# Kernel optimization log

Measured on AMD Instinct MI355X. Metric: run time of the kernel, lower is better.

The kernel has to match this reference:

```python
import jax, jax.numpy as jnp
import numpy as np

N = 100000
E = 500000
HID = 256
N_EDGE_TYPES = 5
N_ATOM = 16
N_CHARGE = 7
NUM_RBF = 16
CUTOFF = 5.0
LN_EPS = 1e-5


def _xavier(key, shape):
    fan_in, fan_out = shape[0], shape[1]
    lim = float(np.sqrt(6.0 / (fan_in + fan_out)))
    return jax.random.uniform(key, shape, jnp.float32, -lim, lim)


def setup_inputs() -> dict:
    key = jax.random.key(0)
    ks = jax.random.split(key, 12)
    input_dim = HID * 2 + NUM_RBF + N_ATOM + N_CHARGE  # 551
    h = jax.random.normal(ks[0], (N, HID), jnp.float32)
    x = jax.random.normal(ks[1], (N, 3), jnp.float32)
    spawn_node_idx = jax.random.randint(ks[2], (E,), 0, N)
    existing_node_idx = jax.random.randint(ks[3], (E,), 0, N)
    ins_x = jax.random.normal(ks[4], (E, 3), jnp.float32)
    ins_a = jax.random.randint(ks[5], (E,), 0, N_ATOM)
    ins_c = jax.random.randint(ks[6], (E,), 0, N_CHARGE)
    # MLP params (Xavier weights, zero biases; LayerNorm gamma=1, beta=0)
    W1 = _xavier(ks[7], (input_dim, HID)); b1 = jnp.zeros((HID,), jnp.float32)
    g1 = jnp.ones((HID,), jnp.float32); be1 = jnp.zeros((HID,), jnp.float32)
    W2 = _xavier(ks[8], (HID, HID // 2)); b2 = jnp.zeros((HID // 2,), jnp.float32)
    g2 = jnp.ones((HID // 2,), jnp.float32); be2 = jnp.zeros((HID // 2,), jnp.float32)
    W3 = _xavier(ks[9], (HID // 2, N_EDGE_TYPES)); b3 = jnp.zeros((N_EDGE_TYPES,), jnp.float32)
    # Gaussian RBF parameters: centers on [0, cutoff], shared width from spacing
    rbf_mu = jnp.linspace(0.0, CUTOFF, NUM_RBF).astype(jnp.float32)
    delta = CUTOFF / (NUM_RBF - 1)
    rbf_gamma = jnp.asarray(1.0 / (2.0 * delta * delta), jnp.float32)
    return {"h": h, "x": x, "spawn_node_idx": spawn_node_idx,
            "existing_node_idx": existing_node_idx, "ins_x": ins_x,
            "ins_a": ins_a, "ins_c": ins_c,
            "W1": W1, "b1": b1, "g1": g1, "be1": be1,
            "W2": W2, "b2": b2, "g2": g2, "be2": be2,
            "W3": W3, "b3": b3, "rbf_mu": rbf_mu, "rbf_gamma": rbf_gamma}


def _layer_norm(z, gamma, beta):
    mu = jnp.mean(z, axis=-1, keepdims=True)
    var = jnp.mean((z - mu) ** 2, axis=-1, keepdims=True)
    return (z - mu) * jax.lax.rsqrt(var + LN_EPS) * gamma + beta


def reference(h, x, spawn_node_idx, existing_node_idx, ins_x, ins_a, ins_c,
              W1, b1, g1, be1, W2, b2, g2, be2, W3, b3, rbf_mu, rbf_gamma):
    # gather node pairs  [E, HID] / [E, 3]
    h_spawn = h[spawn_node_idx]
    h_existing = h[existing_node_idx]
    existing_pos = x[existing_node_idx]
    # distance + Gaussian RBF  [E, NUM_RBF]
    d = jnp.maximum(jnp.linalg.norm(ins_x - existing_pos, axis=-1), 1e-6)
    dist_features = jnp.exp(-rbf_gamma * (d[:, None] - rbf_mu) ** 2)
    # one-hot insertion type features
    ins_atom = jax.nn.one_hot(ins_a, N_ATOM, dtype=h.dtype)
    ins_charge = jax.nn.one_hot(ins_c, N_CHARGE, dtype=h.dtype)
    feats = jnp.concatenate([h_spawn, h_existing, dist_features, ins_atom, ins_charge], axis=-1)
    # 3-layer MLP: Linear -> LN -> SiLU -> Linear -> LN -> SiLU -> Linear
    z = jax.nn.silu(_layer_norm(feats @ W1 + b1, g1, be1))
    z = jax.nn.silu(_layer_norm(z @ W2 + b2, g2, be2))
    return z @ W3 + b3  # [E, N_EDGE_TYPES]
```

## Files before the change

### kernel.cpp

```cpp
#include <hip/hip_runtime.h>
#include <stdint.h>

#define NN 100000
#define EE 500000
#define HIDD 256
#define LN_EPS 1e-5f

typedef _Float16 half8 __attribute__((ext_vector_type(8)));
typedef _Float16 half4 __attribute__((ext_vector_type(4)));
typedef __fp16 fp16x2 __attribute__((ext_vector_type(2)));
typedef float f32x4 __attribute__((ext_vector_type(4)));

__device__ __forceinline__ unsigned short f2h(float f) {
  _Float16 h = (_Float16)f;
  union { _Float16 hh; unsigned short us; } u; u.hh = h;
  return u.us;
}

__device__ __forceinline__ unsigned pkrtz(float a, float b) {
  union { fp16x2 h; unsigned u; } c;
  c.h = __builtin_amdgcn_cvt_pkrtz(a, b);
  return c.u;
}

__device__ __forceinline__ float fast_silu(float y) {
  float e = __expf(-y);
  return y * __builtin_amdgcn_rcpf(1.f + e);
}

__device__ __forceinline__ void g2l16(void* lds, const void* g) {
  __builtin_amdgcn_global_load_lds(
      (const __attribute__((address_space(1))) unsigned int*)g,
      (__attribute__((address_space(3))) unsigned int*)lds, 16, 0, 0);
}

__global__ __launch_bounds__(256) void prep_kern(const float* __restrict__ h,
                                                 const float* __restrict__ W1,
                                                 const float* __restrict__ W2,
                                                 const float* __restrict__ W3,
                                                 unsigned short* __restrict__ hb,
                                                 unsigned short* __restrict__ w1sw,
                                                 unsigned short* __restrict__ w2sw,
                                                 unsigned short* __restrict__ w3sw) {
  int b = blockIdx.x;
  if (b < 712) {
    int t = b * 256 + threadIdx.x;
    if (t < 147456) {
      int chunk = t >> 14, rem = t & 16383;
      int kq = rem >> 11, n = (rem >> 3) & 255, j = rem & 7;
      int k = (chunk << 6) + (kq << 3) + j;
      float v = (k < 551) ? W1[k * 256 + n] : 0.f;
      w1sw[t] = f2h(v);
    } else if (t < 147456 + 32768) {
      int t2 = t - 147456;
      int chunk = t2 >> 13, rem = t2 & 8191;
      int kq = rem >> 10, n = (rem >> 3) & 127, j = rem & 7;
      int k = (chunk << 6) + (kq << 3) + j;
      w2sw[t2] = f2h(W2[k * 128 + n]);
    } else if (t < 147456 + 32768 + 2048) {
      int t3 = t - 180224;
      int kq = t3 >> 7, o = (t3 >> 3) & 15, j = t3 & 7;
      int k = (kq << 3) + j;
      w3sw[t3] = f2h((o < 5) ? W3[k * 5 + o] : 0.f);
    }
  } else {
    int i = ((b - 712) * 256 + threadIdx.x) * 8;
    float4 v0 = *(const float4*)(h + i);
    float4 v1 = *(const float4*)(h + i + 4);
    uint4 u;
    u.x = pkrtz(v0.x, v0.y); u.y = pkrtz(v0.z, v0.w);
    u.z = pkrtz(v1.x, v1.y); u.w = pkrtz(v1.z, v1.w);
    *(uint4*)(hb + i) = u;
  }
}

struct __align__(16) SMem {
  short r1[16384];
  short r2[8192];
  _Float16 b1h[256], g1h[256], be1h[256];
  _Float16 b2h[128], g2h[128], be2h[128];
  float muv[16];
  float b3v[8];
  int spI[64], exI[64];
};

__global__ __launch_bounds__(256, 3)
void edge_head_main(const float* __restrict__ h, const float* __restrict__ x,
                    const int* __restrict__ spawn, const int* __restrict__ exist,
                    const float* __restrict__ insx, const int* __restrict__ insa,
                    const int* __restrict__ insc,
                    const float* __restrict__ b1, const float* __restrict__ g1,
                    const float* __restrict__ be1,
                    const float* __restrict__ b2, const float* __restrict__ g2,
                    const float* __restrict__ be2,
                    const float* __restrict__ b3, const float* __restrict__ mu,
                    const float* __restrict__ gammaP,
                    const unsigned short* __restrict__ w1sw,
                    const unsigned short* __restrict__ w2sw,
                    const unsigned short* __restrict__ w3swg,
                    const unsigned short* __restrict__ hb, int use_hb,
                    float* __restrict__ out) {
  __shared__ SMem sm;
  float* red = (float*)sm.r2;
  const int t = threadIdx.x;
  const int base = blockIdx.x * 64;
  const int lane = t & 63;
  const int wv = t >> 6;
  const int cl = lane & 15;
  const int q = lane >> 4;
  const int sx = (cl & 7) << 3;

  sm.b1h[t] = (_Float16)b1[t]; sm.g1h[t] = (_Float16)g1[t]; sm.be1h[t] = (_Float16)be1[t];
  if (t < 128) { sm.b2h[t] = (_Float16)b2[t]; sm.g2h[t] = (_Float16)g2[t]; sm.be2h[t] = (_Float16)be2[t]; }
  if (t < 16) sm.muv[t] = mu[t];
  if (t < 8) sm.b3v[t] = (t < 5) ? b3[t] : 0.f;
  if (t < 64) {
    int e = base + t; int ec = e < EE ? e : EE - 1;
    sm.spI[t] = spawn[ec]; sm.exI[t] = exist[ec];
  }
  const float gma = gammaP[0];

  __syncthreads();

  int4 f8a = {0,0,0,0}, f8b = {0,0,0,0};
  int k1 = 16, k2 = 32;
  if (t < 64) {
    int e = base + t; int ec = e < EE ? e : EE - 1;
    float ix0 = insx[ec * 3], ix1 = insx[ec * 3 + 1], ix2 = insx[ec * 3 + 2];
    int nd = sm.exI[t];
    float dx = ix0 - x[nd * 3], dy = ix1 - x[nd * 3 + 1], dz = ix2 - x[nd * 3 + 2];
    float d = fmaxf(sqrtf(dx * dx + dy * dy + dz * dz), 1e-6f);
    k1 = 16 + insa[ec]; k2 = 32 + insc[ec];
    float rb[16];
#pragma unroll
    for (int k = 0; k < 16; ++k) { float dd = d - sm.muv[k]; rb[k] = __expf(-gma * dd * dd); }
    uint4 ua, ub;
    ua.x = pkrtz(rb[0], rb[1]);  ua.y = pkrtz(rb[2], rb[3]);
    ua.z = pkrtz(rb[4], rb[5]);  ua.w = pkrtz(rb[6], rb[7]);
    ub.x = pkrtz(rb[8], rb[9]);  ub.y = pkrtz(rb[10], rb[11]);
    ub.z = pkrtz(rb[12], rb[13]); ub.w = pkrtz(rb[14], rb[15]);
    f8a = *(int4*)&ua; f8b = *(int4*)&ub;
  }

  const int row0 = t >> 3, p0 = t & 7;
  const int row1 = row0 + 32;
  const int sw0 = ((p0 ^ (row0 & 7)) << 3);
  const int sw1 = ((p0 ^ (row1 & 7)) << 3);

  int4 pA, pB;
  if (use_hb) {
    pA = *(const int4*)(hb + (size_t)sm.spI[row0] * HIDD + p0 * 8);
    pB = *(const int4*)(hb + (size_t)sm.spI[row1] * HIDD + p0 * 8);
  }

  f32x4 acc[4][4];
#pragma unroll
  for (int i = 0; i < 4; ++i)
#pragma unroll
    for (int j = 0; j < 4; ++j) acc[i][j] = (f32x4){0.f, 0.f, 0.f, 0.f};

  for (int c = 0; c < 9; ++c) {
    __syncthreads();
    const unsigned short* gsrc = w1sw + c * 16384;
#pragma unroll
    for (int i = 0; i < 8; ++i)
      g2l16(&sm.r1[(i * 256 + t) * 8], gsrc + (i * 256 + t) * 8);
    if (c < 8) {
      if (use_hb) {
        *(int4*)&sm.r2[row0 * 64 + sw0] = pA;
        *(int4*)&sm.r2[row1 * 64 + sw1] = pB;
        if (c < 7) {
          const int cn = c + 1;
          const int* sel = (cn < 4) ? sm.spI : sm.exI;
          const int colb = (cn & 3) * 64;
          pA = *(const int4*)(hb + (size_t)sel[row0] * HIDD + colb + p0 * 8);
          pB = *(const int4*)(hb + (size_t)sel[row1] * HIDD + colb + p0 * 8);
        }
      } else {
        const int* sel = (c < 4) ? sm.spI : sm.exI;
        const int colb = (c & 3) * 64;
#pragma unroll
        for (int i = 0; i < 2; ++i) {
          int jj = t + i * 256;
          int row = jj >> 3, p = jj & 7;
          const float* s = h + (size_t)sel[row] * HIDD + colb + p * 8;
          float4 v0 = *(const float4*)s, v1 = *(const float4*)(s + 4);
          uint4 u;
          u.x = pkrtz(v0.x, v0.y); u.y = pkrtz(v0.z, v0.w);
          u.z = pkrtz(v1.x, v1.y); u.w = pkrtz(v1.z, v1.w);
          *(uint4*)&sm.r2[row * 64 + ((p ^ (row & 7)) << 3)] = u;
        }
      }
    } else {
      if (t < 64) {
        short* rp = &sm.r2[t * 64];
        const int sw = t & 7;
#pragma unroll
        for (int g = 0; g < 8; ++g) {
          int4 v = (g == 0) ? f8a : (g == 1) ? f8b : (int4){0,0,0,0};
          *(int4*)&rp[(g ^ sw) * 8] = v;
        }
        rp[((k1 >> 3) ^ sw) * 8 + (k1 & 7)] = (short)0x3C00;
        rp[((k2 >> 3) ^ sw) * 8 + (k2 & 7)] = (short)0x3C00;
      }
    }
    __syncthreads();
#pragma unroll
    for (int ks = 0; ks < 2; ++ks) {
      half8 af[4], bf[4];
#pragma unroll
      for (int i = 0; i < 4; ++i)
        af[i] = *(const half8*)&sm.r1[(ks * 4 + q) * 2048 + (wv * 64 + i * 16 + cl) * 8];
#pragma unroll
      for (int j = 0; j < 4; ++j)
        bf[j] = *(const half8*)&sm.r2[(j * 16 + cl) * 64 + ((ks * 32 + q * 8) ^ sx)];
#pragma unroll
      for (int i = 0; i < 4; ++i)
#pragma unroll
        for (int j = 0; j < 4; ++j)
          acc[i][j] = __builtin_amdgcn_mfma_f32_16x16x32_f16(af[i], bf[j], acc[i][j], 0, 0, 0);
    }
  }

  float bf1[4][4];
#pragma unroll
  for (int i = 0; i < 4; ++i) {
    half4 b4 = *(const half4*)&sm.b1h[wv * 64 + i * 16 + q * 4];
#pragma unroll
    for (int r = 0; r < 4; ++r) bf1[i][r] = (float)b4[r];
  }
  float S1arr[4], Q1arr[4];
#pragma unroll
  for (int j = 0; j < 4; ++j) {
    float S = 0.f, Q = 0.f;
#pragma unroll
    for (int i = 0; i < 4; ++i)
#pragma unroll
      for (int r = 0; r < 4; ++r) {
        float v = acc[i][j][r] + bf1[i][r];
        acc[i][j][r] = v; S += v; Q += v * v;
      }
    S += __shfl_xor(S, 16); S += __shfl_xor(S, 32);
    Q += __shfl_xor(Q, 16); Q += __shfl_xor(Q, 32);
    S1arr[j] = S; Q1arr[j] = Q;
  }
  __syncthreads();
  if (q == 0) {
#pragma unroll
    for (int j = 0; j < 4; ++j) {
      red[wv * 64 + j * 16 + cl] = S1arr[j];
      red[256 + wv * 64 + j * 16 + cl] = Q1arr[j];
    }
  }
  __syncthreads();
  float mean1[4], rstd1[4];
#pragma unroll
  for (int j = 0; j < 4; ++j) {
    int m = j * 16 + cl;
    float S = red[m] + red[64 + m] + red[128 + m] + red[192 + m];
    float Q = red[256 + m] + red[320 + m] + red[384 + m] + red[448 + m];
    float mn = S * (1.f / 256.f);
    mean1[j] = mn;
    rstd1[j] = rsqrtf(Q * (1.f / 256.f) - mn * mn + LN_EPS);
  }
#pragma unroll
  for (int i = 0; i < 4; ++i) {
    half4 g4 = *(const half4*)&sm.g1h[wv * 64 + i * 16 + q * 4];
    half4 e4 = *(const half4*)&sm.be1h[wv * 64 + i * 16 + q * 4];
    float gf[4], ef[4];
#pragma unroll
    for (int r = 0; r < 4; ++r) { gf[r] = (float)g4[r]; ef[r] = (float)e4[r]; }
#pragma unroll
    for (int j = 0; j < 4; ++j) {
      float s0 = fast_silu((acc[i][j][0] - mean1[j]) * rstd1[j] * gf[0] + ef[0]);
      float s1 = fast_silu((acc[i][j][1] - mean1[j]) * rstd1[j] * gf[1] + ef[1]);
      float s2 = fast_silu((acc[i][j][2] - mean1[j]) * rstd1[j] * gf[2] + ef[2]);
      float s3 = fast_silu((acc[i][j][3] - mean1[j]) * rstd1[j] * gf[3] + ef[3]);
      uint2 w; w.x = pkrtz(s0, s1); w.y = pkrtz(s2, s3);
      int m = j * 16 + cl;
      int k0 = wv * 64 + i * 16 + q * 4;
      *(uint2*)&sm.r1[m * 256 + (k0 ^ ((m & 7) << 3))] = w;
    }
  }

  f32x4 acc2[2][4];
#pragma unroll
  for (int i = 0; i < 2; ++i)
#pragma unroll
    for (int j = 0; j < 4; ++j) acc2[i][j] = (f32x4){0.f, 0.f, 0.f, 0.f};
  for (int c2 = 0; c2 < 4; ++c2) {
    __syncthreads();
    const unsigned short* gsrc = w2sw + c2 * 8192;
#pragma unroll
    for (int i = 0; i < 4; ++i)
      g2l16(&sm.r2[(i * 256 + t) * 8], gsrc + (i * 256 + t) * 8);
    __syncthreads();
#pragma unroll
    for (int ks = 0; ks < 2; ++ks) {
      half8 af[2], bf[4];
#pragma unroll
      for (int i = 0; i < 2; ++i)
        af[i] = *(const half8*)&sm.r2[(ks * 4 + q) * 1024 + (wv * 32 + i * 16 + cl) * 8];
#pragma unroll
      for (int j = 0; j < 4; ++j)
        bf[j] = *(const half8*)&sm.r1[(j * 16 + cl) * 256 + ((c2 * 64 + ks * 32 + q * 8) ^ sx)];
#pragma unroll
      for (int i = 0; i < 2; ++i)
#pragma unroll
        for (int j = 0; j < 4; ++j)
          acc2[i][j] = __builtin_amdgcn_mfma_f32_16x16x32_f16(af[i], bf[j], acc2[i][j], 0, 0, 0);
    }
  }
  __syncthreads();

  g2l16(&sm.r1[2048 + t * 8], w3swg + t * 8);

  float bf2[2][4];
#pragma unroll
  for (int i = 0; i < 2; ++i) {
    half4 b4 = *(const half4*)&sm.b2h[wv * 32 + i * 16 + q * 4];
#pragma unroll
    for (int r = 0; r < 4; ++r) bf2[i][r] = (float)b4[r];
  }
  float S2arr[4], Q2arr[4];
#pragma unroll
  for (int j = 0; j < 4; ++j) {
    float S = 0.f, Q = 0.f;
#pragma unroll
    for (int i = 0; i < 2; ++i)
#pragma unroll
      for (int r = 0; r < 4; ++r) {
        float v = acc2[i][j][r] + bf2[i][r];
        acc2[i][j][r] = v; S += v; Q += v * v;
      }
    S += __shfl_xor(S, 16); S += __shfl_xor(S, 32);
    Q += __shfl_xor(Q, 16); Q += __shfl_xor(Q, 32);
    S2arr[j] = S; Q2arr[j] = Q;
  }
  if (q == 0) {
#pragma unroll
    for (int j = 0; j < 4; ++j) {
      red[wv * 64 + j * 16 + cl] = S2arr[j];
      red[256 + wv * 64 + j * 16 + cl] = Q2arr[j];
    }
  }
  __syncthreads();
  float mean2[4], rstd2[4];
#pragma unroll
  for (int j = 0; j < 4; ++j) {
    int m = j * 16 + cl;
    float S = red[m] + red[64 + m] + red[128 + m] + red[192 + m];
    float Q = red[256 + m] + red[320 + m] + red[384 + m] + red[448 + m];
    float mn = S * (1.f / 128.f);
    mean2[j] = mn;
    rstd2[j] = rsqrtf(Q * (1.f / 128.f) - mn * mn + LN_EPS);
  }
  __syncthreads();
#pragma unroll
  for (int i = 0; i < 2; ++i) {
    half4 g4 = *(const half4*)&sm.g2h[wv * 32 + i * 16 + q * 4];
    half4 e4 = *(const half4*)&sm.be2h[wv * 32 + i * 16 + q * 4];
    float gf[4], ef[4];
#pragma unroll
    for (int r = 0; r < 4; ++r) { gf[r] = (float)g4[r]; ef[r] = (float)e4[r]; }
#pragma unroll
    for (int j = 0; j < 4; ++j) {
      float s0 = fast_silu((acc2[i][j][0] - mean2[j]) * rstd2[j] * gf[0] + ef[0]);
      float s1 = fast_silu((acc2[i][j][1] - mean2[j]) * rstd2[j] * gf[1] + ef[1]);
      float s2 = fast_silu((acc2[i][j][2] - mean2[j]) * rstd2[j] * gf[2] + ef[2]);
      float s3 = fast_silu((acc2[i][j][3] - mean2[j]) * rstd2[j] * gf[3] + ef[3]);
      uint2 w; w.x = pkrtz(s0, s1); w.y = pkrtz(s2, s3);
      int m = j * 16 + cl;
      int k0 = wv * 32 + i * 16 + q * 4;
      *(uint2*)&sm.r2[m * 128 + (k0 ^ ((m & 7) << 3))] = w;
    }
  }
  __syncthreads();

  f32x4 a3 = (f32x4){0.f, 0.f, 0.f, 0.f};
  const int m3 = wv * 16 + cl;
  const int sx3 = (m3 & 7) << 3;
#pragma unroll
  for (int ks = 0; ks < 4; ++ks) {
    half8 af = *(const half8*)&sm.r1[2048 + (ks * 4 + q) * 128 + cl * 8];
    half8 bf = *(const half8*)&sm.r2[m3 * 128 + ((ks * 32 + q * 8) ^ sx3)];
    a3 = __builtin_amdgcn_mfma_f32_16x16x32_f16(af, bf, a3, 0, 0, 0);
  }
  int e = base + m3;
  if (e < EE) {
#pragma unroll
    for (int r = 0; r < 4; ++r) {
      int o = q * 4 + r;
      if (o < 5) out[e * 5 + o] = a3[r] + sm.b3v[o];
    }
  }
}

extern "C" void kernel_launch(void* const* d_in, const int* in_sizes, int n_in,
                              void* d_out, int out_size, void* d_ws, size_t ws_size,
                              hipStream_t stream) {
  const float* h    = (const float*)d_in[0];
  const float* x    = (const float*)d_in[1];
  const int* spawn  = (const int*)d_in[2];
  const int* exist  = (const int*)d_in[3];
  const float* insx = (const float*)d_in[4];
  const int* insa   = (const int*)d_in[5];
  const int* insc   = (const int*)d_in[6];
  const float* W1   = (const float*)d_in[7];
  const float* b1   = (const float*)d_in[8];
  const float* g1   = (const float*)d_in[9];
  const float* be1  = (const float*)d_in[10];
  const float* W2   = (const float*)d_in[11];
  const float* b2   = (const float*)d_in[12];
  const float* g2   = (const float*)d_in[13];
  const float* be2  = (const float*)d_in[14];
  const float* W3   = (const float*)d_in[15];
  const float* b3   = (const float*)d_in[16];
  const float* mu   = (const float*)d_in[17];
  const float* gma  = (const float*)d_in[18];

  unsigned short* w1sw = (unsigned short*)d_ws;
  unsigned short* w2sw = w1sw + 147456;
  unsigned short* w3sw = w2sw + 32768;
  unsigned short* hb   = w3sw + 2048;
  const size_t need_hb = 364544ull + (size_t)NN * HIDD * 2ull;
  int use_hb = (ws_size >= need_hb) ? 1 : 0;

  prep_kern<<<use_hb ? 13212 : 712, 256, 0, stream>>>(h, W1, W2, W3, hb, w1sw, w2sw, w3sw);
  edge_head_main<<<7813, 256, 0, stream>>>(h, x, spawn, exist, insx, insa, insc,
                                           b1, g1, be1, b2, g2, be2, b3, mu, gma,
                                           w1sw, w2sw, w3sw, hb, use_hb,
                                           (float*)d_out);
}
```

Before: 463.2 us.

## Load MLP weights directly into registers and double-buffer gathered features in LDS

The swizzled fp16 weights for layers 1, 2 and 3 are now loaded straight from global memory into register fragments rather than staged through LDS with global_load_lds. The layer-1 weight chunk is prefetched one iteration ahead. The gathered activation tiles are double-buffered in LDS so there is one barrier per chunk instead of two. Barriers are replaced by a custom lgkmcnt-wait plus s_barrier macro, and LDS use shrinks because the second buffer is no longer needed. In exchange, every wave re-reads weights from global memory or L2 and register pressure rises under the 3-block occupancy target.

```diff
diff --git a/kernel.cpp b/kernel.cpp
--- a/kernel.cpp
+++ b/kernel.cpp
@@ -11,6 +11,8 @@
 typedef __fp16 fp16x2 __attribute__((ext_vector_type(2)));
 typedef float f32x4 __attribute__((ext_vector_type(4)));
 
+#define LBAR() asm volatile("s_waitcnt lgkmcnt(0)\n\ts_barrier" ::: "memory")
+
 __device__ __forceinline__ unsigned short f2h(float f) {
   _Float16 h = (_Float16)f;
   union { _Float16 hh; unsigned short us; } u; u.hh = h;
@@ -28,10 +30,8 @@
   return y * __builtin_amdgcn_rcpf(1.f + e);
 }
 
-__device__ __forceinline__ void g2l16(void* lds, const void* g) {
-  __builtin_amdgcn_global_load_lds(
-      (const __attribute__((address_space(1))) unsigned int*)g,
-      (__attribute__((address_space(3))) unsigned int*)lds, 16, 0, 0);
+__device__ __forceinline__ half8 ldg8(const unsigned short* p) {
+  return *(const half8*)p;
 }
 
 __global__ __launch_bounds__(256) void prep_kern(const float* __restrict__ h,
@@ -76,7 +76,7 @@
 
 struct __align__(16) SMem {
   short r1[16384];
-  short r2[8192];
+  float red[512];
   _Float16 b1h[256], g1h[256], be1h[256];
   _Float16 b2h[128], g2h[128], be2h[128];
   float muv[16];
@@ -101,7 +101,6 @@
                     const unsigned short* __restrict__ hb, int use_hb,
                     float* __restrict__ out) {
   __shared__ SMem sm;
-  float* red = (float*)sm.r2;
   const int t = threadIdx.x;
   const int base = blockIdx.x * 64;
   const int lane = t & 63;
@@ -120,7 +119,7 @@
   }
   const float gma = gammaP[0];
 
-  __syncthreads();
+  LBAR();
 
   int4 f8a = {0,0,0,0}, f8b = {0,0,0,0};
   int k1 = 16, k2 = 32;
@@ -151,7 +150,41 @@
   if (use_hb) {
     pA = *(const int4*)(hb + (size_t)sm.spI[row0] * HIDD + p0 * 8);
     pB = *(const int4*)(hb + (size_t)sm.spI[row1] * HIDD + p0 * 8);
-  }
+  } else {
+    const float* sA = h + (size_t)sm.spI[row0] * HIDD + p0 * 8;
+    const float* sB = h + (size_t)sm.spI[row1] * HIDD + p0 * 8;
+    float4 a0 = *(const float4*)sA, a1 = *(const float4*)(sA + 4);
+    float4 b0 = *(const float4*)sB, b1v_ = *(const float4*)(sB + 4);
+    uint4 ua, ub;
+    ua.x = pkrtz(a0.x, a0.y); ua.y = pkrtz(a0.z, a0.w); ua.z = pkrtz(a1.x, a1.y); ua.w = pkrtz(a1.z, a1.w);
+    ub.x = pkrtz(b0.x, b0.y); ub.y = pkrtz(b0.z, b0.w); ub.z = pkrtz(b1v_.x, b1v_.y); ub.w = pkrtz(b1v_.z, b1v_.w);
+    pA = *(int4*)&ua; pB = *(int4*)&ub;
+  }
+  *(int4*)&sm.r1[row0 * 64 + sw0] = pA;
+  *(int4*)&sm.r1[row1 * 64 + sw1] = pB;
+  if (use_hb) {
+    pA = *(const int4*)(hb + (size_t)sm.spI[row0] * HIDD + 64 + p0 * 8);
+    pB = *(const int4*)(hb + (size_t)sm.spI[row1] * HIDD + 64 + p0 * 8);
+  } else {
+    const float* sA = h + (size_t)sm.spI[row0] * HIDD + 64 + p0 * 8;
+    const float* sB = h + (size_t)sm.spI[row1] * HIDD + 64 + p0 * 8;
+    float4 a0 = *(const float4*)sA, a1 = *(const float4*)(sA + 4);
+    float4 b0 = *(const float4*)sB, b1v_ = *(const float4*)(sB + 4);
+    uint4 ua, ub;
+    ua.x = pkrtz(a0.x, a0.y); ua.y = pkrtz(a0.z, a0.w); ua.z = pkrtz(a1.x, a1.y); ua.w = pkrtz(a1.z, a1.w);
+    ub.x = pkrtz(b0.x, b0.y); ub.y = pkrtz(b0.z, b0.w); ub.z = pkrtz(b1v_.x, b1v_.y); ub.w = pkrtz(b1v_.z, b1v_.w);
+    pA = *(int4*)&ua; pB = *(int4*)&ub;
+  }
+
+  const unsigned short* w1p = w1sw + q * 2048 + wv * 512 + cl * 8;
+  half8 fcur[8], fnext[8];
+#pragma unroll
+  for (int ks = 0; ks < 2; ++ks)
+#pragma unroll
+    for (int i = 0; i < 4; ++i)
+      fcur[ks * 4 + i] = ldg8(w1p + ks * 8192 + i * 128);
+
+  LBAR();
 
   f32x4 acc[4][4];
 #pragma unroll
@@ -159,67 +192,67 @@
 #pragma unroll
     for (int j = 0; j < 4; ++j) acc[i][j] = (f32x4){0.f, 0.f, 0.f, 0.f};
 
+#pragma unroll
   for (int c = 0; c < 9; ++c) {
-    __syncthreads();
-    const unsigned short* gsrc = w1sw + c * 16384;
-#pragma unroll
-    for (int i = 0; i < 8; ++i)
-      g2l16(&sm.r1[(i * 256 + t) * 8], gsrc + (i * 256 + t) * 8);
-    if (c < 8) {
-      if (use_hb) {
-        *(int4*)&sm.r2[row0 * 64 + sw0] = pA;
-        *(int4*)&sm.r2[row1 * 64 + sw1] = pB;
-        if (c < 7) {
-          const int cn = c + 1;
-          const int* sel = (cn < 4) ? sm.spI : sm.exI;
-          const int colb = (cn & 3) * 64;
+    if (c < 7) {
+      const int nb = ((c + 1) & 1) * 4096;
+      *(int4*)&sm.r1[nb + row0 * 64 + sw0] = pA;
+      *(int4*)&sm.r1[nb + row1 * 64 + sw1] = pB;
+      if (c < 6) {
+        const int cn = c + 2;
+        const int* sel = (cn < 4) ? sm.spI : sm.exI;
+        const int colb = (cn & 3) * 64;
+        if (use_hb) {
           pA = *(const int4*)(hb + (size_t)sel[row0] * HIDD + colb + p0 * 8);
           pB = *(const int4*)(hb + (size_t)sel[row1] * HIDD + colb + p0 * 8);
-        }
-      } else {
-        const int* sel = (c < 4) ? sm.spI : sm.exI;
-        const int colb = (c & 3) * 64;
-#pragma unroll
-        for (int i = 0; i < 2; ++i) {
-          int jj = t + i * 256;
-          int row = jj >> 3, p = jj & 7;
-          const float* s = h + (size_t)sel[row] * HIDD + colb + p * 8;
-          float4 v0 = *(const float4*)s, v1 = *(const float4*)(s + 4);
-          uint4 u;
-          u.x = pkrtz(v0.x, v0.y); u.y = pkrtz(v0.z, v0.w);
-          u.z = pkrtz(v1.x, v1.y); u.w = pkrtz(v1.z, v1.w);
-          *(uint4*)&sm.r2[row * 64 + ((p ^ (row & 7)) << 3)] = u;
+        } else {
+          const float* sA = h + (size_t)sel[row0] * HIDD + colb + p0 * 8;
+          const float* sB = h + (size_t)sel[row1] * HIDD + colb + p0 * 8;
+          float4 a0 = *(const float4*)sA, a1 = *(const float4*)(sA + 4);
+          float4 b0 = *(const float4*)sB, b1v_ = *(const float4*)(sB + 4);
+          uint4 ua, ub;
+          ua.x = pkrtz(a0.x, a0.y); ua.y = pkrtz(a0.z, a0.w); ua.z = pkrtz(a1.x, a1.y); ua.w = pkrtz(a1.z, a1.w);
+          ub.x = pkrtz(b0.x, b0.y); ub.y = pkrtz(b0.z, b0.w); ub.z = pkrtz(b1v_.x, b1v_.y); ub.w = pkrtz(b1v_.z, b1v_.w);
+          pA = *(int4*)&ua; pB = *(int4*)&ub;
         }
       }
-    } else {
+    } else if (c == 7) {
       if (t < 64) {
-        short* rp = &sm.r2[t * 64];
+        short* rp = &sm.r1[t * 64];
         const int sw = t & 7;
 #pragma unroll
         for (int g = 0; g < 8; ++g) {
-          int4 v = (g == 0) ? f8a : (g == 1) ? f8b : (int4){0,0,0,0};
+          int4 v = (g == 0) ? f8a : (g == 1) ? f8b : (int4){0, 0, 0, 0};
           *(int4*)&rp[(g ^ sw) * 8] = v;
         }
         rp[((k1 >> 3) ^ sw) * 8 + (k1 & 7)] = (short)0x3C00;
         rp[((k2 >> 3) ^ sw) * 8 + (k2 & 7)] = (short)0x3C00;
       }
     }
-    __syncthreads();
+    if (c < 8) {
+      const unsigned short* wp = w1p + (c + 1) * 16384;
+#pragma unroll
+      for (int ks = 0; ks < 2; ++ks)
+#pragma unroll
+        for (int i = 0; i < 4; ++i)
+          fnext[ks * 4 + i] = ldg8(wp + ks * 8192 + i * 128);
+    }
+    const int cb = (c & 1) * 4096;
 #pragma unroll
     for (int ks = 0; ks < 2; ++ks) {
-      half8 af[4], bf[4];
+      half8 bf[4];
+#pragma unroll
+      for (int j = 0; j < 4; ++j)
+        bf[j] = *(const half8*)&sm.r1[cb + (j * 16 + cl) * 64 + ((ks * 32 + q * 8) ^ sx)];
 #pragma unroll
       for (int i = 0; i < 4; ++i)
-        af[i] = *(const half8*)&sm.r1[(ks * 4 + q) * 2048 + (wv * 64 + i * 16 + cl) * 8];
-#pragma unroll
-      for (int j = 0; j < 4; ++j)
-        bf[j] = *(const half8*)&sm.r2[(j * 16 + cl) * 64 + ((ks * 32 + q * 8) ^ sx)];
-#pragma unroll
-      for (int i = 0; i < 4; ++i)
 #pragma unroll
         for (int j = 0; j < 4; ++j)
-          acc[i][j] = __builtin_amdgcn_mfma_f32_16x16x32_f16(af[i], bf[j], acc[i][j], 0, 0, 0);
-    }
+          acc[i][j] = __builtin_amdgcn_mfma_f32_16x16x32_f16(fcur[ks * 4 + i], bf[j], acc[i][j], 0, 0, 0);
+    }
+#pragma unroll
+    for (int u = 0; u < 8; ++u) fcur[u] = fnext[u];
+    LBAR();
   }
 
   float bf1[4][4];
@@ -244,21 +277,20 @@
     Q += __shfl_xor(Q, 16); Q += __shfl_xor(Q, 32);
     S1arr[j] = S; Q1arr[j] = Q;
   }
-  __syncthreads();
   if (q == 0) {
 #pragma unroll
     for (int j = 0; j < 4; ++j) {
-      red[wv * 64 + j * 16 + cl] = S1arr[j];
-      red[256 + wv * 64 + j * 16 + cl] = Q1arr[j];
-    }
-  }
-  __syncthreads();
+      sm.red[wv * 64 + j * 16 + cl] = S1arr[j];
+      sm.red[256 + wv * 64 + j * 16 + cl] = Q1arr[j];
+    }
+  }
+  LBAR();
   float mean1[4], rstd1[4];
 #pragma unroll
   for (int j = 0; j < 4; ++j) {
     int m = j * 16 + cl;
-    float S = red[m] + red[64 + m] + red[128 + m] + red[192 + m];
-    float Q = red[256 + m] + red[320 + m] + red[384 + m] + red[448 + m];
+    float S = sm.red[m] + sm.red[64 + m] + sm.red[128 + m] + sm.red[192 + m];
+    float Q = sm.red[256 + m] + sm.red[320 + m] + sm.red[384 + m] + sm.red[448 + m];
     float mn = S * (1.f / 256.f);
     mean1[j] = mn;
     rstd1[j] = rsqrtf(Q * (1.f / 256.f) - mn * mn + LN_EPS);
@@ -282,38 +314,36 @@
       *(uint2*)&sm.r1[m * 256 + (k0 ^ ((m & 7) << 3))] = w;
     }
   }
-
+  LBAR();
+
+  half8 af3[4];
+#pragma unroll
+  for (int ks = 0; ks < 4; ++ks)
+    af3[ks] = ldg8(w3swg + (ks * 4 + q) * 128 + cl * 8);
+
+  const unsigned short* w2p = w2sw + q * 1024 + wv * 256 + cl * 8;
   f32x4 acc2[2][4];
 #pragma unroll
   for (int i = 0; i < 2; ++i)
 #pragma unroll
     for (int j = 0; j < 4; ++j) acc2[i][j] = (f32x4){0.f, 0.f, 0.f, 0.f};
+#pragma unroll
   for (int c2 = 0; c2 < 4; ++c2) {
-    __syncthreads();
-    const unsigned short* gsrc = w2sw + c2 * 8192;
-#pragma unroll
-    for (int i = 0; i < 4; ++i)
-      g2l16(&sm.r2[(i * 256 + t) * 8], gsrc + (i * 256 + t) * 8);
-    __syncthreads();
 #pragma unroll
     for (int ks = 0; ks < 2; ++ks) {
-      half8 af[2], bf[4];
-#pragma unroll
-      for (int i = 0; i < 2; ++i)
-        af[i] = *(const half8*)&sm.r2[(ks * 4 + q) * 1024 + (wv * 32 + i * 16 + cl) * 8];
+      half8 a0 = ldg8(w2p + c2 * 8192 + ks * 4096);
+      half8 a1 = ldg8(w2p + c2 * 8192 + ks * 4096 + 128);
+      half8 bf[4];
 #pragma unroll
       for (int j = 0; j < 4; ++j)
         bf[j] = *(const half8*)&sm.r1[(j * 16 + cl) * 256 + ((c2 * 64 + ks * 32 + q * 8) ^ sx)];
 #pragma unroll
-      for (int i = 0; i < 2; ++i)
-#pragma unroll
-        for (int j = 0; j < 4; ++j)
-          acc2[i][j] = __builtin_amdgcn_mfma_f32_16x16x32_f16(af[i], bf[j], acc2[i][j], 0, 0, 0);
-    }
-  }
-  __syncthreads();
-
-  g2l16(&sm.r1[2048 + t * 8], w3swg + t * 8);
+      for (int j = 0; j < 4; ++j) {
+        acc2[0][j] = __builtin_amdgcn_mfma_f32_16x16x32_f16(a0, bf[j], acc2[0][j], 0, 0, 0);
+        acc2[1][j] = __builtin_amdgcn_mfma_f32_16x16x32_f16(a1, bf[j], acc2[1][j], 0, 0, 0);
+      }
+    }
+  }
 
   float bf2[2][4];
 #pragma unroll
@@ -340,22 +370,21 @@
   if (q == 0) {
 #pragma unroll
     for (int j = 0; j < 4; ++j) {
-      red[wv * 64 + j * 16 + cl] = S2arr[j];
-      red[256 + wv * 64 + j * 16 + cl] = Q2arr[j];
-    }
-  }
-  __syncthreads();
+      sm.red[wv * 64 + j * 16 + cl] = S2arr[j];
+      sm.red[256 + wv * 64 + j * 16 + cl] = Q2arr[j];
+    }
+  }
+  LBAR();
   float mean2[4], rstd2[4];
 #pragma unroll
   for (int j = 0; j < 4; ++j) {
     int m = j * 16 + cl;
-    float S = red[m] + red[64 + m] + red[128 + m] + red[192 + m];
-    float Q = red[256 + m] + red[320 + m] + red[384 + m] + red[448 + m];
+    float S = sm.red[m] + sm.red[64 + m] + sm.red[128 + m] + sm.red[192 + m];
+    float Q = sm.red[256 + m] + sm.red[320 + m] + sm.red[384 + m] + sm.red[448 + m];
     float mn = S * (1.f / 128.f);
     mean2[j] = mn;
     rstd2[j] = rsqrtf(Q * (1.f / 128.f) - mn * mn + LN_EPS);
   }
-  __syncthreads();
 #pragma unroll
   for (int i = 0; i < 2; ++i) {
     half4 g4 = *(const half4*)&sm.g2h[wv * 32 + i * 16 + q * 4];
@@ -372,19 +401,18 @@
       uint2 w; w.x = pkrtz(s0, s1); w.y = pkrtz(s2, s3);
       int m = j * 16 + cl;
       int k0 = wv * 32 + i * 16 + q * 4;
-      *(uint2*)&sm.r2[m * 128 + (k0 ^ ((m & 7) << 3))] = w;
-    }
-  }
-  __syncthreads();
+      *(uint2*)&sm.r1[m * 128 + (k0 ^ ((m & 7) << 3))] = w;
+    }
+  }
+  LBAR();
 
   f32x4 a3 = (f32x4){0.f, 0.f, 0.f, 0.f};
   const int m3 = wv * 16 + cl;
   const int sx3 = (m3 & 7) << 3;
 #pragma unroll
   for (int ks = 0; ks < 4; ++ks) {
-    half8 af = *(const half8*)&sm.r1[2048 + (ks * 4 + q) * 128 + cl * 8];
-    half8 bf = *(const half8*)&sm.r2[m3 * 128 + ((ks * 32 + q * 8) ^ sx3)];
-    a3 = __builtin_amdgcn_mfma_f32_16x16x32_f16(af, bf, a3, 0, 0, 0);
+    half8 bf = *(const half8*)&sm.r1[m3 * 128 + ((ks * 32 + q * 8) ^ sx3)];
+    a3 = __builtin_amdgcn_mfma_f32_16x16x32_f16(af3[ks], bf, a3, 0, 0, 0);
   }
   int e = base + m3;
   if (e < EE) {
```

Measured after the change: 418.3 us. 9.7% less time.
